# Kernel optimization log

Measured on AMD Instinct MI355X. Metric: run time of the kernel, lower is better.

## Reference

```python
import jax, jax.numpy as jnp
import numpy as np

B, T, N, CIN, H, K, HOR = 64, 12, 800, 2, 64, 3, 12
TCOV_IN, TCOV_H, MNUM, MDIM = 60, 2, 4, 8
KAPPA = 0.05
IN0 = CIN + TCOV_H  # layer-0 input dim: data channels + time-covariate embedding


def setup_inputs() -> dict:
    key = jax.random.key(0)
    ks = jax.random.split(key, 24)
    def nrm(k, shape, s=0.1):
        return jax.random.normal(k, shape, jnp.float32) * s
    inp = {}
    inp["x_seq"] = jax.random.normal(ks[0], (B, T, N, CIN), jnp.float32)
    inp["t_x"] = jax.random.normal(ks[1], (B, T, TCOV_IN), jnp.float32)
    inp["t_y"] = jax.random.normal(ks[2], (B, HOR, TCOV_IN), jnp.float32)
    # adaptive graph as in init_adp_graph: softmax(relu(v1 @ v2), axis=1)
    inp["G"] = jax.nn.softmax(jax.nn.relu(nrm(ks[3], (N, 20), 1.0) @ nrm(ks[4], (20, N), 1.0)), axis=1)
    i = 5
    for pre in ("enc", "dec"):
        for l, hin in enumerate((IN0, H)):
            inp[f"{pre}_Wg{l}"] = nrm(ks[i], ((hin + H) * K, 2 * H)); i += 1
            inp[f"{pre}_bg{l}"] = jnp.zeros((2 * H,), jnp.float32)
            inp[f"{pre}_Wc{l}"] = nrm(ks[i], ((hin + H) * K, H)); i += 1
            inp[f"{pre}_bc{l}"] = jnp.zeros((H,), jnp.float32)
    inp["mlp_W1"] = nrm(ks[i], (TCOV_IN, 10)); i += 1
    inp["mlp_b1"] = jnp.zeros((10,), jnp.float32)
    inp["mlp_W2"] = nrm(ks[i], (10, TCOV_H * N)); i += 1
    inp["mlp_b2"] = jnp.zeros((TCOV_H * N,), jnp.float32)
    inp["memory"] = nrm(ks[i], (MNUM, MDIM), 1.0); i += 1
    inp["Wa"] = nrm(ks[i], (N * H, MDIM), 0.01); i += 1
    inp["fc"] = nrm(ks[i], (MDIM, MDIM * N), 0.1); i += 1
    inp["proj_W"] = nrm(ks[i], (H + MDIM, CIN)); i += 1
    inp["proj_b"] = jnp.zeros((CIN,), jnp.float32)
    return inp


def _cheby(G):
    # Chebyshev basis T_0..T_{K-1}: T_0=I, T_1=G, T_k = 2 G T_{k-1} - T_{k-2}
    Gs = [jnp.eye(N, dtype=G.dtype), G]
    for _ in range(2, K):
        Gs.append(2.0 * (G @ Gs[-1]) - Gs[-2])
    return jnp.stack(Gs[:K])  # (K, N, N)


def _gconv(x, Gs, W, b):
    # mixhop: h_k = kappa*x + (1-kappa) * einsum('bnp,nm->bmp', x, T_k); concat over k, then project
    agg = KAPPA * x[None] + (1.0 - KAPPA) * jnp.einsum('bnp,knm->kbmp', x, Gs)  # (K,B,N,P)
    Bq, Nq, P = x.shape
    h = jnp.transpose(agg, (1, 2, 0, 3)).reshape(Bq, Nq, K * P)  # matches torch.cat order
    return h @ W + b


def _cell(x, h, Gs, Wg, bg, Wc, bc):
    # GCRU cell: graph-conv GRU
    ur = _gconv(jnp.concatenate([x, h], -1), Gs, Wg, bg)
    u, r = jnp.split(ur, 2, axis=-1)
    u = jax.nn.sigmoid(u)
    r = jax.nn.sigmoid(r)
    c = jnp.tanh(_gconv(jnp.concatenate([x, r * h], -1), Gs, Wc, bc))
    return (1.0 - u) * h + u * c


def _mlp(t, W1, b1, W2, b2):
    # nn.Sequential(Linear, Linear) -- no activation in between
    return (t @ W1 + b1) @ W2 + b2


def reference(x_seq, t_x, t_y, G, enc_Wg0, enc_bg0, enc_Wc0, enc_bc0, enc_Wg1, enc_bg1, enc_Wc1, enc_bc1, dec_Wg0, dec_bg0, dec_Wc0, dec_bc0, dec_Wg1, dec_bg1, dec_Wc1, dec_bc1, mlp_W1, mlp_b1, mlp_W2, mlp_b2, memory, Wa, fc, proj_W, proj_b):
    Gs = _cheby(G)
    # time covariates for encoder input
    tx_emb = _mlp(t_x, mlp_W1, mlp_b1, mlp_W2, mlp_b2).reshape(B, T, N, TCOV_H)
    x = jnp.concatenate([x_seq, tx_emb], -1)  # (B,T,N,IN0)
    # encoder: scan over time per layer
    seq = jnp.swapaxes(x, 0, 1)  # (T,B,N,.)
    enc_params = [(enc_Wg0, enc_bg0, enc_Wc0, enc_bc0), (enc_Wg1, enc_bg1, enc_Wc1, enc_bc1)]
    h_last = []
    for (Wg, bg, Wc, bc) in enc_params:
        def step(h, xt, Wg=Wg, bg=bg, Wc=Wc, bc=bc):
            hn = _cell(xt, h, Gs, Wg, bg, Wc, bc)
            return hn, hn
        h0 = jnp.zeros((B, N, H), x.dtype)
        hT, seq = jax.lax.scan(step, h0, seq)
        h_last.append(hT)
    dec_params = [(dec_Wg0, dec_bg0, dec_Wc0, dec_bc0), (dec_Wg1, dec_bg1, dec_Wc1, dec_bc1)]
    ty = jnp.swapaxes(t_y, 0, 1)  # (HOR,B,TCOV_IN)

    def dec_step(carry, tyt):
        go, h0, h1 = carry
        tye = _mlp(tyt, mlp_W1, mlp_b1, mlp_W2, mlp_b2).reshape(B, N, TCOV_H)
        xin = jnp.concatenate([go, tye], -1)
        h0 = _cell(xin, h0, Gs, *dec_params[0])
        h1 = _cell(h0, h1, Gs, *dec_params[1])
        # query_st_memory
        q = h1.reshape(B, N * H) @ Wa  # (B, MDIM)
        att = jax.nn.softmax(q @ memory.T, axis=1)  # (B, MNUM)
        attm = ((att @ memory) @ fc).reshape(B, N, MDIM)
        out = jax.nn.relu(jnp.concatenate([h1, attm], -1) @ proj_W + proj_b)  # (B,N,CIN)
        return (out, h0, h1), out

    go0 = jnp.zeros((B, N, CIN), x.dtype)
    _, outs = jax.lax.scan(dec_step, (go0, h_last[0], h_last[1]), ty)
    return jnp.swapaxes(outs, 0, 1)  # (B,HOR,N,CIN)
```

## Files before the change

### kernel.cpp

```cpp
#include <hip/hip_runtime.h>
#include <math.h>

typedef _Float16 f16_t;
typedef _Float16 half8 __attribute__((ext_vector_type(8)));
typedef float f32x4 __attribute__((ext_vector_type(4)));


struct Params {
  const float *x_seq, *t_x, *t_y, *G;
  const float *Wraw[8], *bia[8];
  const float *mW1, *mb1, *mW2, *mb2, *mem, *Wa, *fc, *projW, *projb;
  float* dout;
  float *h0, *h1, *txe, *tye, *hidb, *partial, *Wat;
  f16_t *T2h, *Bpk;
  f16_t *Y0gL[2], *YbgL[2], *Y0cL[2], *YbcL[2], *UhL[2];
  f16_t* wsp[8];
};

__device__ __forceinline__ float sigm(float x) { return 1.0f / (1.0f + expf(-x)); }

__device__ __forceinline__ int xcd_swz(int orig, int nwg) {
  int q = nwg >> 3, r = nwg & 7, xcd = orig & 7, j = orig >> 3;
  return (xcd < r ? xcd * (q + 1) : r * (q + 1) + (xcd - r) * q) + j;
}

__device__ __forceinline__ void gload16(const void* g, void* l) {
  __builtin_amdgcn_global_load_lds((const __attribute__((address_space(1))) void*)g,
                                   (__attribute__((address_space(3))) void*)l, 16, 0, 0);
}


__global__ void __launch_bounds__(256) k_pre0(Params p) {
  int nt = gridDim.x * blockDim.x, id = blockIdx.x * blockDim.x + threadIdx.x;
  float4 z = {0.f, 0.f, 0.f, 0.f};
  for (int i = id; i < 64 * 64 * 200; i += nt) { ((float4*)p.h0)[i] = z; ((float4*)p.h1)[i] = z; }
  for (int w = 0; w < 8; ++w) {
    int layer = (w >> 1) & 1, cand = w & 1;
    int P = layer ? 128 : 68, NC = cand ? 64 : 128;
    const float* W = p.Wraw[w];
    f16_t* dst = p.wsp[w];
    int tot = 3 * NC * 128;
    for (int idx = id; idx < tot; idx += nt) {
      int s = idx / (NC * 128), rem = idx - s * (NC * 128);
      int c = rem >> 7, pp = rem & 127;
      float v = 0.f;
      if (pp < P) {
        if (s == 0)
          v = W[(size_t)pp * NC + c] + 0.05f * (W[(size_t)(P + pp) * NC + c] + W[(size_t)(2 * P + pp) * NC + c]);
        else
          v = 0.95f * W[(size_t)(s * P + pp) * NC + c];
      }
      dst[idx] = (f16_t)v;
    }
  }
  for (int idx = id; idx < 15360; idx += nt) {
    int half = idx / 7680, rem = idx - half * 7680;
    int r = rem / 10, j = rem - r * 10;
    const float* tin = half ? p.t_y : p.t_x;
    float a = p.mb1[j];
    for (int k = 0; k < 60; ++k) a += tin[(size_t)r * 60 + k] * p.mW1[k * 10 + j];
    p.hidb[idx] = a;
  }
  for (int idx = id; idx < 409600; idx += nt) {
    int c = idx / 6400, r2 = idx - c * 6400;
    int n = r2 >> 3, d = r2 & 7;
    p.Wat[idx] = p.Wa[((size_t)n * 64 + c) * 8 + d];
  }
}

__global__ void __launch_bounds__(256) k_pre1(Params p) {
  __shared__ float As[16 * 68];
  __shared__ float Bs[16 * 68];
  int tid = threadIdx.x, tx = tid & 15, ty = tid >> 4;
  const float* A = p.G;
  for (int tile = blockIdx.x; tile < 169; tile += gridDim.x) {
    int bx = tile % 13, by = tile / 13;
    int rowBase = by * 64, colBase = bx * 64;
    float acc[4][4] = {};
    for (int k0 = 0; k0 < 800; k0 += 16) {
      __syncthreads();
      for (int e = tid; e < 1024; e += 256) {
        int r = e >> 4, c = e & 15;
        int gr = rowBase + r;
        As[c * 68 + r] = (gr < 800) ? A[gr * 800 + k0 + c] : 0.f;
      }
      for (int e = tid; e < 1024; e += 256) {
        int r = e >> 6, c = e & 63;
        int gc = colBase + c;
        Bs[r * 68 + c] = (gc < 800) ? A[(k0 + r) * 800 + gc] : 0.f;
      }
      __syncthreads();
#pragma unroll
      for (int kk = 0; kk < 16; ++kk) {
        float4 a4 = *(const float4*)&As[kk * 68 + ty * 4];
        float4 b4 = *(const float4*)&Bs[kk * 68 + tx * 4];
        float av[4] = {a4.x, a4.y, a4.z, a4.w};
        float bv[4] = {b4.x, b4.y, b4.z, b4.w};
#pragma unroll
        for (int i = 0; i < 4; ++i)
#pragma unroll
          for (int j = 0; j < 4; ++j) acc[i][j] += av[i] * bv[j];
      }
    }
#pragma unroll
    for (int i = 0; i < 4; ++i) {
      int m = rowBase + ty * 4 + i;
      if (m >= 800) continue;
#pragma unroll
      for (int j = 0; j < 4; ++j) {
        int n = colBase + tx * 4 + j;
        if (n < 800) p.T2h[(size_t)m * 800 + n] = (f16_t)(2.f * acc[i][j] - (m == n ? 1.f : 0.f));
      }
    }
  }
  int nt = gridDim.x * blockDim.x, id = blockIdx.x * blockDim.x + threadIdx.x;
  for (int idx = id; idx < 2 * 768 * 1600; idx += nt) {
    int half = idx / (768 * 1600), rem = idx - half * (768 * 1600);
    int r = rem / 1600, o = rem - r * 1600;
    const float* hid = p.hidb + half * 7680;
    float* emb = half ? p.tye : p.txe;
    float a = p.mb2[o];
#pragma unroll
    for (int k = 0; k < 10; ++k) a += hid[r * 10 + k] * p.mW2[k * 1600 + o];
    emb[rem] = a;
  }
}

__global__ void __launch_bounds__(256) k_pre2(Params p) {
  int nt = gridDim.x * blockDim.x, id = blockIdx.x * blockDim.x + threadIdx.x;
  for (int idx = id; idx < 7 * 50 * 4096; idx += nt) {
    int nT = idx / 204800, rem = idx - nT * 204800;
    int ks = rem >> 12, i = rem & 4095;
    int kg = i >> 10, col = (i >> 3) & 127, e = i & 7;
    int k = ks * 32 + kg * 8 + e;
    int n = nT * 128 + col;
    f16_t v = (f16_t)0.f;
    if (n < 800) v = (k < 800) ? (f16_t)p.G[(size_t)k * 800 + n] : p.T2h[(size_t)(k - 800) * 800 + n];
    p.Bpk[idx] = v;
  }
}

template <int LAYER>
__device__ void small_body(const Params& p, char* smraw, int widx, int dec, int t,
                           f16_t* __restrict__ Y0g, f16_t* __restrict__ Ybg, int lblk) {
  f16_t* XS = (f16_t*)smraw;
  unsigned* XS32 = (unsigned*)smraw;
  int tid = threadIdx.x, lane = tid & 63, wid = tid >> 6;
  int lrow = lane & 15, lgrp = lane >> 4;
  int wm = wid >> 1, wn = wid & 1;
  int swz = xcd_swz(lblk, 448);
  int b = swz / 7, nBase = (swz % 7) * 128;
  const f16_t* __restrict__ wb = p.wsp[widx];
  const float* emb = dec ? p.tye : p.txe;

  {
    int rp = tid >> 3, n0 = (tid & 7) * 16;
    int ng = nBase + n0;
    bool nval = ng < 800;
    for (int pass = 0; pass < 2; ++pass) {
      float v[2][16];
#pragma unroll
      for (int par = 0; par < 2; ++par) {
        int cp = pass * 64 + 2 * rp + par;
        float* vv = v[par];
        if (!nval) {
#pragma unroll
          for (int i = 0; i < 16; ++i) vv[i] = 0.f;
        } else if (LAYER == 1) {
          const float* src = (cp < 64) ? p.h0 + ((size_t)(b * 64 + cp)) * 800 + ng
                                       : p.h1 + ((size_t)(b * 64 + cp - 64)) * 800 + ng;
#pragma unroll
          for (int q = 0; q < 4; ++q) {
            float4 f = *(const float4*)(src + q * 4);
            vv[q * 4 + 0] = f.x; vv[q * 4 + 1] = f.y; vv[q * 4 + 2] = f.z; vv[q * 4 + 3] = f.w;
          }
        } else {
          if (cp >= 68) {
#pragma unroll
            for (int i = 0; i < 16; ++i) vv[i] = 0.f;
          } else if (cp >= 4) {
            const float* src = p.h0 + ((size_t)(b * 64 + cp - 4)) * 800 + ng;
#pragma unroll
            for (int q = 0; q < 4; ++q) {
              float4 f = *(const float4*)(src + q * 4);
              vv[q * 4 + 0] = f.x; vv[q * 4 + 1] = f.y; vv[q * 4 + 2] = f.z; vv[q * 4 + 3] = f.w;
            }
          } else if (cp >= 2) {
#pragma unroll
            for (int i = 0; i < 16; ++i)
              vv[i] = emb[(size_t)(b * 12 + t) * 1600 + (ng + i) * 2 + (cp - 2)];
          } else {
            if (dec) {
              if (t == 0) {
#pragma unroll
                for (int i = 0; i < 16; ++i) vv[i] = 0.f;
              } else {
#pragma unroll
                for (int i = 0; i < 16; ++i)
                  vv[i] = p.dout[((size_t)(b * 12 + t - 1) * 800 + ng + i) * 2 + cp];
              }
            } else {
#pragma unroll
              for (int i = 0; i < 16; ++i)
                vv[i] = p.x_seq[((size_t)(b * 12 + t) * 800 + ng + i) * 2 + cp];
            }
          }
        }
      }
#pragma unroll
      for (int i = 0; i < 16; ++i) {
        union { f16_t h[2]; unsigned u; } pk;
        pk.h[0] = (f16_t)v[0][i];
        pk.h[1] = (f16_t)v[1][i];
        XS32[(n0 + i) * 68 + pass * 32 + rp] = pk.u;
      }
    }
  }
  __syncthreads();

  for (int s = 0; s < 3; ++s) {
    f32x4 acc[4][4];
#pragma unroll
    for (int i = 0; i < 4; ++i)
#pragma unroll
      for (int j = 0; j < 4; ++j) acc[i][j] = (f32x4){0.f, 0.f, 0.f, 0.f};
#pragma unroll
    for (int ks = 0; ks < 4; ++ks) {
      half8 fa[4], fx[4];
#pragma unroll
      for (int mf = 0; mf < 4; ++mf)
        fa[mf] = *(const half8*)(wb + ((size_t)(s * 128 + wm * 64 + mf * 16 + lrow) << 7) + ks * 32 + lgrp * 8);
#pragma unroll
      for (int nt = 0; nt < 4; ++nt)
        fx[nt] = *(const half8*)(XS + (wn * 64 + nt * 16 + lrow) * 136 + ks * 32 + lgrp * 8);
#pragma unroll
      for (int mf = 0; mf < 4; ++mf)
#pragma unroll
        for (int nt = 0; nt < 4; ++nt)
          acc[mf][nt] = __builtin_amdgcn_mfma_f32_16x16x32_f16(fa[mf], fx[nt], acc[mf][nt], 0, 0, 0);
    }
#pragma unroll
    for (int mf = 0; mf < 4; ++mf)
#pragma unroll
      for (int nt = 0; nt < 4; ++nt) {
        int n = nBase + wn * 64 + nt * 16 + lrow;
        if (n >= 800) continue;
#pragma unroll
        for (int j = 0; j < 4; ++j) {
          int c = wm * 64 + mf * 16 + lgrp * 4 + j;
          size_t r = (size_t)(b * 128 + c);
          f16_t val = (f16_t)acc[mf][nt][j];
          if (s == 0) {
            Y0g[r * 800 + n] = val;
          } else {
            int kp = (s - 1) * 800 + n;
            Ybg[((size_t)(kp >> 3) * 8192 + r) * 8 + (kp & 7)] = val;
          }
        }
      }
  }
}

template <int LAYER>
__device__ void biggate_body(const Params& p, char* smraw, int w0, int dec, int t, float* hcur,
                             const f16_t* __restrict__ Y0g, const f16_t* __restrict__ Ybg,
                             f16_t* __restrict__ Y0c, f16_t* __restrict__ Ybc,
                             f16_t* __restrict__ Uh, int lblk) {
  constexpr int Pin = LAYER ? 64 : 4;
  f16_t* SH = (f16_t*)smraw;
  f16_t* AS = SH;
  f16_t* BS = SH + 6144;
  int tid = threadIdx.x, lane = tid & 63, w = tid >> 6;
  int lrow = lane & 15, lgrp = lane >> 4;
  int wm = w >> 1, wn = w & 1;
  int swz = xcd_swz(lblk, 896);
  int rt = swz / 7;
  int rBase = rt * 64;
  int nTile = swz % 7;
  int b = rt >> 1;
  int rhblk = rt & 1;
  const f16_t* __restrict__ Bbase = p.Bpk + (size_t)nTile * 204800;
  const float* bias = p.bia[w0];

  auto stage = [&](int buf, int ks) {
    gload16(Ybg + ((size_t)(ks * 4 + w) * 8192 + rBase + lane) * 8, AS + buf * 2048 + w * 512);
    gload16(Bbase + (size_t)ks * 4096 + (size_t)(w * 2 + 0) * 512 + lane * 8, BS + buf * 4096 + (w * 2 + 0) * 512);
    gload16(Bbase + (size_t)ks * 4096 + (size_t)(w * 2 + 1) * 512 + lane * 8, BS + buf * 4096 + (w * 2 + 1) * 512);
  };

  f32x4 acc[2][4];
#pragma unroll
  for (int i = 0; i < 2; ++i)
#pragma unroll
    for (int j = 0; j < 4; ++j) acc[i][j] = (f32x4){0.f, 0.f, 0.f, 0.f};

  stage(0, 0);
  stage(1, 1);
  for (int ks = 0; ks < 50; ++ks) {
    if (ks == 49) {
      asm volatile("s_waitcnt vmcnt(0)" ::: "memory");
    } else {
      asm volatile("s_waitcnt vmcnt(3)" ::: "memory");
    }
    __builtin_amdgcn_s_barrier();
    __builtin_amdgcn_sched_barrier(0);
    if (ks + 2 < 50) stage((ks + 2) % 3, ks + 2);
    int cur = ks % 3;
    half8 fa[2], fb[4];
#pragma unroll
    for (int mt = 0; mt < 2; ++mt)
      fa[mt] = *(const half8*)(AS + cur * 2048 + lgrp * 512 + (wm * 32 + mt * 16 + lrow) * 8);
#pragma unroll
    for (int nt = 0; nt < 4; ++nt)
      fb[nt] = *(const half8*)(BS + cur * 4096 + lgrp * 1024 + (wn * 64 + nt * 16 + lrow) * 8);
#pragma unroll
    for (int mt = 0; mt < 2; ++mt)
#pragma unroll
      for (int nt = 0; nt < 4; ++nt)
        acc[mt][nt] = __builtin_amdgcn_mfma_f32_16x16x32_f16(fa[mt], fb[nt], acc[mt][nt], 0, 0, 0);
  }

  if (!rhblk) {
#pragma unroll
    for (int mt = 0; mt < 2; ++mt)
#pragma unroll
      for (int nt = 0; nt < 4; ++nt) {
        int n = nTile * 128 + wn * 64 + nt * 16 + lrow;
        if (n >= 800) continue;
#pragma unroll
        for (int j = 0; j < 4; ++j) {
          int c = wm * 32 + mt * 16 + lgrp * 4 + j;
          int r = rBase + c;
          float v = acc[mt][nt][j] + (float)Y0g[(size_t)r * 800 + n] + bias[c];
          Uh[(size_t)(b * 64 + c) * 800 + n] = (f16_t)sigm(v);
        }
      }
    return;
  }

  f16_t rhv[2][4][4];
#pragma unroll
  for (int mt = 0; mt < 2; ++mt)
#pragma unroll
    for (int nt = 0; nt < 4; ++nt) {
      int n = nTile * 128 + wn * 64 + nt * 16 + lrow;
#pragma unroll
      for (int j = 0; j < 4; ++j) {
        int jj = wm * 32 + mt * 16 + lgrp * 4 + j;
        if (n < 800) {
          int r = rBase + jj;
          float v = acc[mt][nt][j] + (float)Y0g[(size_t)r * 800 + n] + bias[64 + jj];
          float hv = hcur[(size_t)(b * 64 + jj) * 800 + n];
          rhv[mt][nt][j] = (f16_t)(sigm(v) * hv);
        } else {
          rhv[mt][nt][j] = (f16_t)0.f;
        }
      }
    }

  __syncthreads();
  f16_t* Xc = SH;

#pragma unroll
  for (int mt = 0; mt < 2; ++mt)
#pragma unroll
    for (int nt = 0; nt < 4; ++nt) {
      int col = wn * 64 + nt * 16 + lrow;
#pragma unroll
      for (int j = 0; j < 4; ++j) {
        int jj = wm * 32 + mt * 16 + lgrp * 4 + j;
        Xc[col * 136 + Pin + jj] = rhv[mt][nt][j];
      }
    }
  if (LAYER == 1) {
    int ct = tid >> 2, nq = tid & 3;
    const float* src = p.h0 + (size_t)(b * 64 + ct) * 800;
#pragma unroll 8
    for (int i = 0; i < 32; ++i) {
      int nl = nq * 32 + i;
      int n = nTile * 128 + nl;
      float v = (n < 800) ? src[n] : 0.f;
      Xc[nl * 136 + ct] = (f16_t)v;
    }
  } else {
    if (tid < 128) {
      int col = tid;
      int n = nTile * 128 + col;
      float v0 = 0.f, v1 = 0.f, v2 = 0.f, v3 = 0.f;
      if (n < 800) {
        if (dec) {
          if (t > 0) {
            v0 = p.dout[((size_t)(b * 12 + t - 1) * 800 + n) * 2 + 0];
            v1 = p.dout[((size_t)(b * 12 + t - 1) * 800 + n) * 2 + 1];
          }
        } else {
          v0 = p.x_seq[((size_t)(b * 12 + t) * 800 + n) * 2 + 0];
          v1 = p.x_seq[((size_t)(b * 12 + t) * 800 + n) * 2 + 1];
        }
        const float* emb = dec ? p.tye : p.txe;
        v2 = emb[(size_t)(b * 12 + t) * 1600 + n * 2 + 0];
        v3 = emb[(size_t)(b * 12 + t) * 1600 + n * 2 + 1];
      }
      Xc[col * 136 + 0] = (f16_t)v0;
      Xc[col * 136 + 1] = (f16_t)v1;
      Xc[col * 136 + 2] = (f16_t)v2;
      Xc[col * 136 + 3] = (f16_t)v3;
      unsigned* z32 = (unsigned*)(Xc + col * 136 + 68);
#pragma unroll
      for (int q = 0; q < 30; ++q) z32[q] = 0u;
    }
  }
  __syncthreads();

  const f16_t* __restrict__ wc = p.wsp[w0 + 1];
  int cwn = w;
  for (int s = 0; s < 3; ++s) {
    f32x4 ac[4][2];
#pragma unroll
    for (int i = 0; i < 4; ++i)
#pragma unroll
      for (int j = 0; j < 2; ++j) ac[i][j] = (f32x4){0.f, 0.f, 0.f, 0.f};
#pragma unroll
    for (int ks = 0; ks < 4; ++ks) {
      half8 fa[4], fx[2];
#pragma unroll
      for (int mf = 0; mf < 4; ++mf)
        fa[mf] = *(const half8*)(wc + ((size_t)(s * 64 + mf * 16 + lrow) << 7) + ks * 32 + lgrp * 8);
#pragma unroll
      for (int nt = 0; nt < 2; ++nt)
        fx[nt] = *(const half8*)(Xc + (cwn * 32 + nt * 16 + lrow) * 136 + ks * 32 + lgrp * 8);
#pragma unroll
      for (int mf = 0; mf < 4; ++mf)
#pragma unroll
        for (int nt = 0; nt < 2; ++nt)
          ac[mf][nt] = __builtin_amdgcn_mfma_f32_16x16x32_f16(fa[mf], fx[nt], ac[mf][nt], 0, 0, 0);
    }
#pragma unroll
    for (int mf = 0; mf < 4; ++mf)
#pragma unroll
      for (int nt = 0; nt < 2; ++nt) {
        int n = nTile * 128 + cwn * 32 + nt * 16 + lrow;
        if (n >= 800) continue;
#pragma unroll
        for (int j = 0; j < 4; ++j) {
          int c = mf * 16 + lgrp * 4 + j;
          size_t r = (size_t)(b * 64 + c);
          f16_t val = (f16_t)ac[mf][nt][j];
          if (s == 0) {
            Y0c[r * 800 + n] = val;
          } else {
            int kp = (s - 1) * 800 + n;
            Ybc[((size_t)(kp >> 3) * 4096 + r) * 8 + (kp & 7)] = val;
          }
        }
      }
  }
}

__device__ void bigcand_body(const Params& p, char* smraw, int widx, float* hcur,
                             const f16_t* __restrict__ Y0c, const f16_t* __restrict__ Ybc,
                             const f16_t* __restrict__ Uh, int lblk) {
  f16_t* SH = (f16_t*)smraw;
  f16_t* AS = SH;
  f16_t* BS = SH + 6144;
  int tid = threadIdx.x, lane = tid & 63, w = tid >> 6;
  int lrow = lane & 15, lgrp = lane >> 4;
  int wm = w >> 1, wn = w & 1;
  int swz = xcd_swz(lblk, 448);
  int rBase = (swz / 7) * 64;
  int nTile = swz % 7;
  const f16_t* __restrict__ Bbase = p.Bpk + (size_t)nTile * 204800;
  const float* bias = p.bia[widx];

  auto stage = [&](int buf, int ks) {
    gload16(Ybc + ((size_t)(ks * 4 + w) * 4096 + rBase + lane) * 8, AS + buf * 2048 + w * 512);
    gload16(Bbase + (size_t)ks * 4096 + (size_t)(w * 2 + 0) * 512 + lane * 8, BS + buf * 4096 + (w * 2 + 0) * 512);
    gload16(Bbase + (size_t)ks * 4096 + (size_t)(w * 2 + 1) * 512 + lane * 8, BS + buf * 4096 + (w * 2 + 1) * 512);
  };

  f32x4 acc[2][4];
#pragma unroll
  for (int i = 0; i < 2; ++i)
#pragma unroll
    for (int j = 0; j < 4; ++j) acc[i][j] = (f32x4){0.f, 0.f, 0.f, 0.f};

  stage(0, 0);
  stage(1, 1);
  for (int ks = 0; ks < 50; ++ks) {
    if (ks == 49) {
      asm volatile("s_waitcnt vmcnt(0)" ::: "memory");
    } else {
      asm volatile("s_waitcnt vmcnt(3)" ::: "memory");
    }
    __builtin_amdgcn_s_barrier();
    __builtin_amdgcn_sched_barrier(0);
    if (ks + 2 < 50) stage((ks + 2) % 3, ks + 2);
    int cur = ks % 3;
    half8 fa[2], fb[4];
#pragma unroll
    for (int mt = 0; mt < 2; ++mt)
      fa[mt] = *(const half8*)(AS + cur * 2048 + lgrp * 512 + (wm * 32 + mt * 16 + lrow) * 8);
#pragma unroll
    for (int nt = 0; nt < 4; ++nt)
      fb[nt] = *(const half8*)(BS + cur * 4096 + lgrp * 1024 + (wn * 64 + nt * 16 + lrow) * 8);
#pragma unroll
    for (int mt = 0; mt < 2; ++mt)
#pragma unroll
      for (int nt = 0; nt < 4; ++nt)
        acc[mt][nt] = __builtin_amdgcn_mfma_f32_16x16x32_f16(fa[mt], fb[nt], acc[mt][nt], 0, 0, 0);
  }

#pragma unroll
  for (int mt = 0; mt < 2; ++mt)
#pragma unroll
    for (int nt = 0; nt < 4; ++nt) {
      int n = nTile * 128 + wn * 64 + nt * 16 + lrow;
      if (n >= 800) continue;
#pragma unroll
      for (int j = 0; j < 4; ++j) {
        int r = rBase + wm * 32 + mt * 16 + lgrp * 4 + j;
        int b = r >> 6, c = r & 63;
        float v = acc[mt][nt][j] + (float)Y0c[(size_t)r * 800 + n] + bias[c];
        float u = (float)Uh[(size_t)(b * 64 + c) * 800 + n];
        float hv = hcur[(size_t)(b * 64 + c) * 800 + n];
        hcur[(size_t)(b * 64 + c) * 800 + n] = (1.f - u) * hv + u * tanhf(v);
      }
    }
}


template <int LAYER>
__global__ void __launch_bounds__(256, 3) s_one(Params p, int widx, int dec, int t) {
  __shared__ __align__(16) char sm[34816];
  small_body<LAYER>(p, sm, widx, dec, t, p.Y0gL[LAYER], p.YbgL[LAYER], blockIdx.x);
}
__global__ void __launch_bounds__(256, 3) s_both(Params p, int t0, int t1) {
  __shared__ __align__(16) char sm[34816];
  if (blockIdx.x < 448)
    small_body<0>(p, sm, 0, 0, t0, p.Y0gL[0], p.YbgL[0], blockIdx.x);
  else
    small_body<1>(p, sm, 2, 0, t1, p.Y0gL[1], p.YbgL[1], blockIdx.x - 448);
}

template <int LAYER>
__global__ void __launch_bounds__(256, 4) gg_one(Params p, int w0, int dec, int t) {
  __shared__ __align__(16) char sm[36864];
  biggate_body<LAYER>(p, sm, w0, dec, t, LAYER ? p.h1 : p.h0, p.Y0gL[LAYER], p.YbgL[LAYER],
                      p.Y0cL[LAYER], p.YbcL[LAYER], p.UhL[LAYER], blockIdx.x);
}
__global__ void __launch_bounds__(256, 4) gg_both(Params p, int t0, int t1) {
  __shared__ __align__(16) char sm[36864];
  if (blockIdx.x < 896)
    biggate_body<0>(p, sm, 0, 0, t0, p.h0, p.Y0gL[0], p.YbgL[0], p.Y0cL[0], p.YbcL[0], p.UhL[0], blockIdx.x);
  else
    biggate_body<1>(p, sm, 2, 0, t1, p.h1, p.Y0gL[1], p.YbgL[1], p.Y0cL[1], p.YbcL[1], p.UhL[1], blockIdx.x - 896);
}

__global__ void __launch_bounds__(256, 4) gc_one(Params p, int widx, int layer) {
  __shared__ __align__(16) char sm[36864];
  bigcand_body(p, sm, widx, layer ? p.h1 : p.h0, p.Y0cL[layer], p.YbcL[layer], p.UhL[layer], blockIdx.x);
}
__global__ void __launch_bounds__(256, 4) gc_both(Params p) {
  __shared__ __align__(16) char sm[36864];
  if (blockIdx.x < 448)
    bigcand_body(p, sm, 1, p.h0, p.Y0cL[0], p.YbcL[0], p.UhL[0], blockIdx.x);
  else
    bigcand_body(p, sm, 3, p.h1, p.Y0cL[1], p.YbcL[1], p.UhL[1], blockIdx.x - 448);
}


__global__ void __launch_bounds__(256) k_att1(Params p) {
  int gwid = (blockIdx.x * blockDim.x + threadIdx.x) >> 6;
  int nw = (gridDim.x * blockDim.x) >> 6;
  int lane = threadIdx.x & 63;
  for (int tile = gwid; tile < 1024; tile += nw) {
    int cx = tile & 15, b = tile >> 4;
    float acc[8] = {};
    const float* hrow = p.h1 + (size_t)b * 51200 + cx * 3200;
    const float* wbase = p.Wat + (size_t)cx * 3200 * 8;
    for (int i = lane; i < 3200; i += 64) {
      float hv = hrow[i];
      const float* wr = wbase + (size_t)i * 8;
#pragma unroll
      for (int j = 0; j < 8; ++j) acc[j] += hv * wr[j];
    }
#pragma unroll
    for (int s = 1; s < 64; s <<= 1) {
#pragma unroll
      for (int j = 0; j < 8; ++j) acc[j] += __shfl_xor(acc[j], s);
    }
    if (lane == 0) {
#pragma unroll
      for (int j = 0; j < 8; ++j) p.partial[((size_t)b * 16 + cx) * 8 + j] = acc[j];
    }
  }
}

__global__ void __launch_bounds__(256) k_att2(Params p, int t) {
  int b = blockIdx.x >> 2, q4 = blockIdx.x & 3;
  int tid = threadIdx.x;
  float qv[8] = {};
  for (int cx = 0; cx < 16; ++cx)
#pragma unroll
    for (int j = 0; j < 8; ++j) qv[j] += p.partial[((size_t)b * 16 + cx) * 8 + j];
  float sco[4], mx = -1e30f;
#pragma unroll
  for (int m = 0; m < 4; ++m) {
    float s = 0.f;
#pragma unroll
    for (int d = 0; d < 8; ++d) s += qv[d] * p.mem[m * 8 + d];
    sco[m] = s;
    mx = fmaxf(mx, s);
  }
  float se = 0.f;
#pragma unroll
  for (int m = 0; m < 4; ++m) { sco[m] = expf(sco[m] - mx); se += sco[m]; }
  float attv[8];
#pragma unroll
  for (int d = 0; d < 8; ++d) {
    float av = 0.f;
#pragma unroll
    for (int m = 0; m < 4; ++m) av += (sco[m] / se) * p.mem[m * 8 + d];
    attv[d] = av;
  }
  if (tid >= 200) return;
  int n = q4 * 200 + tid;
  float attm[8];
#pragma unroll
  for (int d = 0; d < 8; ++d) {
    float s = 0.f;
#pragma unroll
    for (int m = 0; m < 8; ++m) s += attv[m] * p.fc[(size_t)m * 6400 + n * 8 + d];
    attm[d] = s;
  }
  float o0 = p.projb[0], o1 = p.projb[1];
  const float* hb = p.h1 + (size_t)b * 51200 + n;
#pragma unroll 16
  for (int j = 0; j < 64; ++j) {
    float hv = hb[(size_t)j * 800];
    o0 += hv * p.projW[j * 2 + 0];
    o1 += hv * p.projW[j * 2 + 1];
  }
#pragma unroll
  for (int d = 0; d < 8; ++d) {
    o0 += attm[d] * p.projW[(64 + d) * 2 + 0];
    o1 += attm[d] * p.projW[(64 + d) * 2 + 1];
  }
  size_t base = ((size_t)(b * 12 + t) * 800 + n) * 2;
  p.dout[base + 0] = fmaxf(o0, 0.f);
  p.dout[base + 1] = fmaxf(o1, 0.f);
}


extern "C" void kernel_launch(void* const* d_in, const int* in_sizes, int n_in,
                              void* d_out, int out_size, void* d_ws, size_t ws_size,
                              hipStream_t stream) {
  Params P;
  P.x_seq = (const float*)d_in[0];
  P.t_x = (const float*)d_in[1];
  P.t_y = (const float*)d_in[2];
  P.G = (const float*)d_in[3];
  P.Wraw[0] = (const float*)d_in[4];  P.bia[0] = (const float*)d_in[5];
  P.Wraw[1] = (const float*)d_in[6];  P.bia[1] = (const float*)d_in[7];
  P.Wraw[2] = (const float*)d_in[8];  P.bia[2] = (const float*)d_in[9];
  P.Wraw[3] = (const float*)d_in[10]; P.bia[3] = (const float*)d_in[11];
  P.Wraw[4] = (const float*)d_in[12]; P.bia[4] = (const float*)d_in[13];
  P.Wraw[5] = (const float*)d_in[14]; P.bia[5] = (const float*)d_in[15];
  P.Wraw[6] = (const float*)d_in[16]; P.bia[6] = (const float*)d_in[17];
  P.Wraw[7] = (const float*)d_in[18]; P.bia[7] = (const float*)d_in[19];
  P.mW1 = (const float*)d_in[20];
  P.mb1 = (const float*)d_in[21];
  P.mW2 = (const float*)d_in[22];
  P.mb2 = (const float*)d_in[23];
  P.mem = (const float*)d_in[24];
  P.Wa = (const float*)d_in[25];
  P.fc = (const float*)d_in[26];
  P.projW = (const float*)d_in[27];
  P.projb = (const float*)d_in[28];
  P.dout = (float*)d_out;

  float* ws = (float*)d_ws;
  size_t off = 0;
  auto alloc = [&](size_t nel) { float* q = ws + off; off += (nel + 3) & ~(size_t)3; return q; };
  P.T2h = (f16_t*)alloc(320000);
  P.Bpk = (f16_t*)alloc((size_t)7 * 50 * 4096 / 2);
  for (int l = 0; l < 2; ++l) {
    P.Y0gL[l] = (f16_t*)alloc((size_t)8192 * 800 / 2);
    P.YbgL[l] = (f16_t*)alloc((size_t)1600 * 8192 / 2);
    P.Y0cL[l] = (f16_t*)alloc((size_t)4096 * 800 / 2);
    P.YbcL[l] = (f16_t*)alloc((size_t)1600 * 4096 / 2);
    P.UhL[l] = (f16_t*)alloc((size_t)4096 * 800 / 2);
  }
  P.h0 = alloc((size_t)4096 * 800);
  P.h1 = alloc((size_t)4096 * 800);
  P.txe = alloc((size_t)768 * 1600);
  P.tye = alloc((size_t)768 * 1600);
  P.hidb = alloc(15360);
  P.partial = alloc(8192);
  P.Wat = alloc(409600);
  for (int w = 0; w < 8; ++w) {
    int cand = w & 1;
    int NC = cand ? 64 : 128;
    P.wsp[w] = (f16_t*)alloc((size_t)3 * NC * 128 / 2);
  }

  k_pre0<<<512, 256, 0, stream>>>(P);
  k_pre1<<<512, 256, 0, stream>>>(P);
  k_pre2<<<512, 256, 0, stream>>>(P);

  s_one<0><<<448, 256, 0, stream>>>(P, 0, 0, 0);
  gg_one<0><<<896, 256, 0, stream>>>(P, 0, 0, 0);
  gc_one<<<448, 256, 0, stream>>>(P, 1, 0);
  for (int s = 1; s <= 11; ++s) {
    s_both<<<896, 256, 0, stream>>>(P, s, s - 1);
    gg_both<<<1792, 256, 0, stream>>>(P, s, s - 1);
    gc_both<<<896, 256, 0, stream>>>(P);
  }
  s_one<1><<<448, 256, 0, stream>>>(P, 2, 0, 11);
  gg_one<1><<<896, 256, 0, stream>>>(P, 2, 0, 11);
  gc_one<<<448, 256, 0, stream>>>(P, 3, 1);

  for (int t = 0; t < 12; ++t) {
    s_one<0><<<448, 256, 0, stream>>>(P, 4, 1, t);
    gg_one<0><<<896, 256, 0, stream>>>(P, 4, 1, t);
    gc_one<<<448, 256, 0, stream>>>(P, 5, 0);
    s_one<1><<<448, 256, 0, stream>>>(P, 6, 1, t);
    gg_one<1><<<896, 256, 0, stream>>>(P, 6, 1, t);
    gc_one<<<448, 256, 0, stream>>>(P, 7, 1);
    k_att1<<<256, 256, 0, stream>>>(P);
    k_att2<<<256, 256, 0, stream>>>(P, t);
  }
}
```

Baseline: 6.471 ms.

## Merge update and reset gate tiles into one 128-row block per batch

The gate GEMM block tile grows from 64 to 128 output rows, so one workgroup computes both the update (u) and reset (r) gate halves for a batch and node tile. The grid halves, and each B-operand tile loaded from the packed graph matrix is reused across twice as many rows, cutting B traffic. Only the r-half warps write r*h into shared memory for the candidate staging. The cost is more accumulator registers, larger LDS (48KB), and occupancy lowered to 3 blocks per CU.

```diff
diff --git a/kernel.cpp b/kernel.cpp
--- a/kernel.cpp
+++ b/kernel.cpp
@@ -269,28 +269,31 @@
   constexpr int Pin = LAYER ? 64 : 4;
   f16_t* SH = (f16_t*)smraw;
   f16_t* AS = SH;
-  f16_t* BS = SH + 6144;
+  f16_t* BS = SH + 12288;
   int tid = threadIdx.x, lane = tid & 63, w = tid >> 6;
   int lrow = lane & 15, lgrp = lane >> 4;
   int wm = w >> 1, wn = w & 1;
-  int swz = xcd_swz(lblk, 896);
-  int rt = swz / 7;
-  int rBase = rt * 64;
+  int swz = xcd_swz(lblk, 448);
+  int b = swz / 7;
+  int rBase = b * 128;
   int nTile = swz % 7;
-  int b = rt >> 1;
-  int rhblk = rt & 1;
   const f16_t* __restrict__ Bbase = p.Bpk + (size_t)nTile * 204800;
   const float* bias = p.bia[w0];
 
   auto stage = [&](int buf, int ks) {
-    gload16(Ybg + ((size_t)(ks * 4 + w) * 8192 + rBase + lane) * 8, AS + buf * 2048 + w * 512);
-    gload16(Bbase + (size_t)ks * 4096 + (size_t)(w * 2 + 0) * 512 + lane * 8, BS + buf * 4096 + (w * 2 + 0) * 512);
-    gload16(Bbase + (size_t)ks * 4096 + (size_t)(w * 2 + 1) * 512 + lane * 8, BS + buf * 4096 + (w * 2 + 1) * 512);
+    const f16_t* asrc = Ybg + ((size_t)(ks * 4 + w) * 8192 + rBase + lane) * 8;
+    f16_t* adst = AS + buf * 4096 + w * 1024 + lane * 8;
+    gload16(asrc, adst);
+    gload16(asrc + 64 * 8, adst + 64 * 8);
+    const f16_t* bsrc = Bbase + (size_t)ks * 4096 + w * 1024 + lane * 8;
+    f16_t* bdst = BS + buf * 4096 + w * 1024 + lane * 8;
+    gload16(bsrc, bdst);
+    gload16(bsrc + 64 * 8, bdst + 64 * 8);
   };
 
-  f32x4 acc[2][4];
-#pragma unroll
-  for (int i = 0; i < 2; ++i)
+  f32x4 acc[4][4];
+#pragma unroll
+  for (int i = 0; i < 4; ++i)
 #pragma unroll
     for (int j = 0; j < 4; ++j) acc[i][j] = (f32x4){0.f, 0.f, 0.f, 0.f};
 
@@ -300,59 +303,46 @@
     if (ks == 49) {
       asm volatile("s_waitcnt vmcnt(0)" ::: "memory");
     } else {
-      asm volatile("s_waitcnt vmcnt(3)" ::: "memory");
+      asm volatile("s_waitcnt vmcnt(4)" ::: "memory");
     }
     __builtin_amdgcn_s_barrier();
     __builtin_amdgcn_sched_barrier(0);
     if (ks + 2 < 50) stage((ks + 2) % 3, ks + 2);
     int cur = ks % 3;
-    half8 fa[2], fb[4];
-#pragma unroll
-    for (int mt = 0; mt < 2; ++mt)
-      fa[mt] = *(const half8*)(AS + cur * 2048 + lgrp * 512 + (wm * 32 + mt * 16 + lrow) * 8);
+    half8 fa[4], fb[4];
+#pragma unroll
+    for (int mt = 0; mt < 4; ++mt)
+      fa[mt] = *(const half8*)(AS + cur * 4096 + lgrp * 1024 + (wm * 64 + mt * 16 + lrow) * 8);
 #pragma unroll
     for (int nt = 0; nt < 4; ++nt)
       fb[nt] = *(const half8*)(BS + cur * 4096 + lgrp * 1024 + (wn * 64 + nt * 16 + lrow) * 8);
 #pragma unroll
-    for (int mt = 0; mt < 2; ++mt)
+    for (int mt = 0; mt < 4; ++mt)
 #pragma unroll
       for (int nt = 0; nt < 4; ++nt)
         acc[mt][nt] = __builtin_amdgcn_mfma_f32_16x16x32_f16(fa[mt], fb[nt], acc[mt][nt], 0, 0, 0);
   }
 
-  if (!rhblk) {
-#pragma unroll
-    for (int mt = 0; mt < 2; ++mt)
-#pragma unroll
-      for (int nt = 0; nt < 4; ++nt) {
-        int n = nTile * 128 + wn * 64 + nt * 16 + lrow;
-        if (n >= 800) continue;
-#pragma unroll
-        for (int j = 0; j < 4; ++j) {
-          int c = wm * 32 + mt * 16 + lgrp * 4 + j;
-          int r = rBase + c;
-          float v = acc[mt][nt][j] + (float)Y0g[(size_t)r * 800 + n] + bias[c];
-          Uh[(size_t)(b * 64 + c) * 800 + n] = (f16_t)sigm(v);
-        }
-      }
-    return;
-  }
-
-  f16_t rhv[2][4][4];
-#pragma unroll
-  for (int mt = 0; mt < 2; ++mt)
+  f16_t rhv[4][4][4];
+#pragma unroll
+  for (int mt = 0; mt < 4; ++mt)
 #pragma unroll
     for (int nt = 0; nt < 4; ++nt) {
       int n = nTile * 128 + wn * 64 + nt * 16 + lrow;
 #pragma unroll
       for (int j = 0; j < 4; ++j) {
-        int jj = wm * 32 + mt * 16 + lgrp * 4 + j;
+        int c = wm * 64 + mt * 16 + lgrp * 4 + j;
+        int r = rBase + c;
         if (n < 800) {
-          int r = rBase + jj;
-          float v = acc[mt][nt][j] + (float)Y0g[(size_t)r * 800 + n] + bias[64 + jj];
-          float hv = hcur[(size_t)(b * 64 + jj) * 800 + n];
-          rhv[mt][nt][j] = (f16_t)(sigm(v) * hv);
-        } else {
+          float v = acc[mt][nt][j] + (float)Y0g[(size_t)r * 800 + n] + bias[c];
+          float sv = sigm(v);
+          if (c < 64) {
+            Uh[(size_t)(b * 64 + c) * 800 + n] = (f16_t)sv;
+          } else {
+            float hv = hcur[(size_t)(b * 64 + (c - 64)) * 800 + n];
+            rhv[mt][nt][j] = (f16_t)(sv * hv);
+          }
+        } else if (c >= 64) {
           rhv[mt][nt][j] = (f16_t)0.f;
         }
       }
@@ -361,17 +351,19 @@
   __syncthreads();
   f16_t* Xc = SH;
 
-#pragma unroll
-  for (int mt = 0; mt < 2; ++mt)
-#pragma unroll
-    for (int nt = 0; nt < 4; ++nt) {
-      int col = wn * 64 + nt * 16 + lrow;
-#pragma unroll
-      for (int j = 0; j < 4; ++j) {
-        int jj = wm * 32 + mt * 16 + lgrp * 4 + j;
-        Xc[col * 136 + Pin + jj] = rhv[mt][nt][j];
-      }
-    }
+  if (wm == 1) {
+#pragma unroll
+    for (int mt = 0; mt < 4; ++mt)
+#pragma unroll
+      for (int nt = 0; nt < 4; ++nt) {
+        int col = wn * 64 + nt * 16 + lrow;
+#pragma unroll
+        for (int j = 0; j < 4; ++j) {
+          int jj = mt * 16 + lgrp * 4 + j;
+          Xc[col * 136 + Pin + jj] = rhv[mt][nt][j];
+        }
+      }
+  }
   if (LAYER == 1) {
     int ct = tid >> 2, nq = tid & 3;
     const float* src = p.h0 + (size_t)(b * 64 + ct) * 800;
@@ -543,17 +535,17 @@
 }
 
 template <int LAYER>
-__global__ void __launch_bounds__(256, 4) gg_one(Params p, int w0, int dec, int t) {
-  __shared__ __align__(16) char sm[36864];
+__global__ void __launch_bounds__(256, 3) gg_one(Params p, int w0, int dec, int t) {
+  __shared__ __align__(16) char sm[49152];
   biggate_body<LAYER>(p, sm, w0, dec, t, LAYER ? p.h1 : p.h0, p.Y0gL[LAYER], p.YbgL[LAYER],
                       p.Y0cL[LAYER], p.YbcL[LAYER], p.UhL[LAYER], blockIdx.x);
 }
-__global__ void __launch_bounds__(256, 4) gg_both(Params p, int t0, int t1) {
-  __shared__ __align__(16) char sm[36864];
-  if (blockIdx.x < 896)
+__global__ void __launch_bounds__(256, 3) gg_both(Params p, int t0, int t1) {
+  __shared__ __align__(16) char sm[49152];
+  if (blockIdx.x < 448)
     biggate_body<0>(p, sm, 0, 0, t0, p.h0, p.Y0gL[0], p.YbgL[0], p.Y0cL[0], p.YbcL[0], p.UhL[0], blockIdx.x);
   else
-    biggate_body<1>(p, sm, 2, 0, t1, p.h1, p.Y0gL[1], p.YbgL[1], p.Y0cL[1], p.YbcL[1], p.UhL[1], blockIdx.x - 896);
+    biggate_body<1>(p, sm, 2, 0, t1, p.h1, p.Y0gL[1], p.YbgL[1], p.Y0cL[1], p.YbcL[1], p.UhL[1], blockIdx.x - 448);
 }
 
 __global__ void __launch_bounds__(256, 4) gc_one(Params p, int widx, int layer) {
@@ -709,23 +701,23 @@
   k_pre2<<<512, 256, 0, stream>>>(P);
 
   s_one<0><<<448, 256, 0, stream>>>(P, 0, 0, 0);
-  gg_one<0><<<896, 256, 0, stream>>>(P, 0, 0, 0);
+  gg_one<0><<<448, 256, 0, stream>>>(P, 0, 0, 0);
   gc_one<<<448, 256, 0, stream>>>(P, 1, 0);
   for (int s = 1; s <= 11; ++s) {
     s_both<<<896, 256, 0, stream>>>(P, s, s - 1);
-    gg_both<<<1792, 256, 0, stream>>>(P, s, s - 1);
+    gg_both<<<896, 256, 0, stream>>>(P, s, s - 1);
     gc_both<<<896, 256, 0, stream>>>(P);
   }
   s_one<1><<<448, 256, 0, stream>>>(P, 2, 0, 11);
-  gg_one<1><<<896, 256, 0, stream>>>(P, 2, 0, 11);
+  gg_one<1><<<448, 256, 0, stream>>>(P, 2, 0, 11);
   gc_one<<<448, 256, 0, stream>>>(P, 3, 1);
 
   for (int t = 0; t < 12; ++t) {
     s_one<0><<<448, 256, 0, stream>>>(P, 4, 1, t);
-    gg_one<0><<<896, 256, 0, stream>>>(P, 4, 1, t);
+    gg_one<0><<<448, 256, 0, stream>>>(P, 4, 1, t);
     gc_one<<<448, 256, 0, stream>>>(P, 5, 0);
     s_one<1><<<448, 256, 0, stream>>>(P, 6, 1, t);
-    gg_one<1><<<896, 256, 0, stream>>>(P, 6, 1, t);
+    gg_one<1><<<448, 256, 0, stream>>>(P, 6, 1, t);
     gc_one<<<448, 256, 0, stream>>>(P, 7, 1);
     k_att1<<<256, 256, 0, stream>>>(P);
     k_att2<<<256, 256, 0, stream>>>(P, t);
```

Result: slower. 6.833 ms (+5.6%).
